# Performance work log

Measured on AMD Instinct MI355X. Metric: run time of the kernel, lower is better.

The kernel has to match this reference:

```python
import jax, jax.numpy as jnp
import numpy as np

B, T, F, C, H = 256, 96, 256, 256, 512
NH, FFD = 8, 64  # transformer nhead=8, dim_feedforward=64 (PyPOTS defaults)


def make_pe(L, d):
    pos = np.arange(L)[:, None].astype(np.float32)
    div = np.exp(np.arange(0, d, 2).astype(np.float32) * (-np.log(10000.0) / d))
    pe = np.zeros((L, d), np.float32)
    pe[:, 0::2] = np.sin(pos * div)
    pe[:, 1::2] = np.cos(pos * div)
    return jnp.asarray(pe)


def setup_inputs() -> dict:
    key = jax.random.key(0)
    it = iter(jax.random.split(key, 64))

    def u(shape):
        s = 1.0 / np.sqrt(shape[-1])
        return jax.random.uniform(next(it), shape, jnp.float32, -s, s)

    return {
        "x": jax.random.normal(next(it), (B, T, F), jnp.float32),
        "mask": (jax.random.uniform(next(it), (B, T, F)) > 0.3).astype(jnp.float32),
        "deltas": jax.random.uniform(next(it), (B, T, F), jnp.float32) * 5.0,
        "last_obs": jax.random.normal(next(it), (B, T, F), jnp.float32),
        "intervals": jax.random.uniform(next(it), (F,), jnp.float32) * 2.0,
        "Wo": u((F, F)), "bo": jnp.zeros(F),            # Decay_obs linear
        "Wip": u((C, F)), "bip": jnp.zeros(C),          # input_projection (k=1 conv)
        "Wqkv": u((3 * C, C)), "bqkv": jnp.zeros(3 * C),
        "Wao": u((C, C)), "bao": jnp.zeros(C),
        "g1": jnp.ones(C), "be1": jnp.zeros(C),
        "W1": u((FFD, C)), "b1": jnp.zeros(FFD),
        "W2": u((C, FFD)), "b2": jnp.zeros(C),
        "g2": jnp.ones(C), "be2": jnp.zeros(C),
        "Wop1": u((H, C)), "bop1": jnp.zeros(H),        # output_projection1
        "wop2": u((2 * T,)), "bop2": jnp.zeros(1),      # output_projection2 (2T->1, k=1)
        "Wdh": u((H, F)), "bdh": jnp.zeros(H),          # temp_decay_h
        "wdx": u((F,)), "bdx": jnp.zeros(F),            # temp_decay_x (diag)
        "Wh": u((F, H)), "bh": jnp.zeros(F),            # hist
        "Wfr": u((F, F)), "bfr": jnp.zeros(F),          # feat_reg_v (off-diag mask)
        "Wwc": u((F, 2 * F)), "bwc": jnp.zeros(F),      # weight_combine
        "Wih": u((3 * H, 2 * F)), "bih": jnp.zeros(3 * H),
        "Whh": u((3 * H, H)), "bhh": jnp.zeros(3 * H),
    }


def layernorm(x, g, b):
    mu = jnp.mean(x, -1, keepdims=True)
    v = jnp.var(x, -1, keepdims=True)
    return (x - mu) * jax.lax.rsqrt(v + 1e-5) * g + b


def _forward(x, mask, deltas, last_obs, intervals, Wo, bo, Wip, bip, Wqkv, bqkv,
             Wao, bao, g1, be1, W1, b1, W2, b2, g2, be2, Wop1, bop1, wop2, bop2,
             Wdh, bdh, wdx, bdx, Wh, bh, Wfr, bfr, Wwc, bwc, Wih, bih, Whh, bhh):
    Bb, Tt, Ff = x.shape
    Cc = Wip.shape[0]
    DH = Cc // NH
    # --- Decay_obs: weight = 0.5 * (1 - tanh(sign(dd) * |W dd + b|)) ---
    dd = deltas - intervals[None, None, :]
    wd = dd @ Wo.T + bo
    decay_factor = 0.5 * (1.0 - jnp.tanh(jnp.sign(dd) * jnp.abs(wd)))
    # --- pre-encoder (h is None path) ---
    pe = make_pe(Tt, Cc)[None]                      # (1, T, C)
    d_lo = last_obs @ Wip.T + bip + pe
    d_df = decay_factor @ Wip.T + bip + pe
    data = jnp.concatenate([d_lo, d_df], axis=1)    # (B, 2T, C)
    # TransformerEncoderLayer(batch_first=False) on (B, 2T, C):
    # seq dim = axis 0 (batch), "batch" dim = axis 1 -- faithful to source quirk.
    qkv = data @ Wqkv.T + bqkv
    q, k, v = jnp.split(qkv, 3, axis=-1)
    q = q.reshape(Bb, 2 * Tt, NH, DH)
    k = k.reshape(Bb, 2 * Tt, NH, DH)
    v = v.reshape(Bb, 2 * Tt, NH, DH)
    scores = jnp.einsum('ilhd,jlhd->lhij', q, k) / float(np.sqrt(DH))
    attn = jax.nn.softmax(scores, axis=-1)
    ctx = jnp.einsum('lhij,jlhd->ilhd', attn, v).reshape(Bb, 2 * Tt, Cc)
    data = layernorm(data + ctx @ Wao.T + bao, g1, be1)
    ff = jax.nn.gelu(data @ W1.T + b1, approximate=False) @ W2.T + b2
    data = layernorm(data + ff, g2, be2)
    data = data @ Wop1.T + bop1                     # (B, 2T, H)
    h0 = jnp.einsum('blh,l->bh', data, wop2) + bop2 # output_projection2 -> (B, H)
    # --- sequential imputation loop ---
    Wfr_m = Wfr * (1.0 - jnp.eye(Ff, dtype=Wfr.dtype))
    def step(h, ts):
        x_t, d_t, m_t = ts
        gamma_h = jnp.exp(-jax.nn.relu(d_t @ Wdh.T + bdh))
        h = h * gamma_h
        x_h = h @ Wh.T + bh
        x_r = m_t * x_t + (1.0 - m_t) * x_h
        xu = x_r @ Wfr_m.T + bfr
        gamma_x = jnp.exp(-jax.nn.relu(d_t * wdx + bdx))
        beta = jnp.concatenate([gamma_x, m_t], axis=-1) @ Wwc.T + bwc
        x_comb = beta * xu + (1.0 - beta) * x_h
        loss = jnp.sum(jnp.abs(x_comb - x_t) * m_t) / (jnp.sum(m_t) + 1e-12)
        x_imp_t = m_t * x_t + (1.0 - m_t) * x_comb
        gi = jnp.concatenate([x_imp_t, m_t], axis=-1) @ Wih.T + bih
        gh = h @ Whh.T + bhh
        ir, iz, inn = jnp.split(gi, 3, axis=-1)
        hr, hz, hn = jnp.split(gh, 3, axis=-1)
        r = jax.nn.sigmoid(ir + hr)
        z = jax.nn.sigmoid(iz + hz)
        n = jnp.tanh(inn + r * hn)
        h_new = (1.0 - z) * n + z * h
        return h_new, (x_imp_t, x_comb, loss)

    xs = (jnp.swapaxes(x, 0, 1), jnp.swapaxes(deltas, 0, 1), jnp.swapaxes(mask, 0, 1))
    h_fin, (xi, rec, losses) = jax.lax.scan(step, h0, xs)
    x_imp = jnp.swapaxes(xi, 0, 1)
    reconstruction = jnp.swapaxes(rec, 0, 1)
    return x_imp, reconstruction, h_fin, jnp.sum(losses)


def reference(x, mask, deltas, last_obs, intervals, Wo, bo, Wip, bip, Wqkv, bqkv,
              Wao, bao, g1, be1, W1, b1, W2, b2, g2, be2, Wop1, bop1, wop2, bop2,
              Wdh, bdh, wdx, bdx, Wh, bh, Wfr, bfr, Wwc, bwc, Wih, bih, Whh, bhh):
    return _forward(x, mask, deltas, last_obs, intervals, Wo, bo, Wip, bip, Wqkv,
                    bqkv, Wao, bao, g1, be1, W1, b1, W2, b2, g2, be2, Wop1, bop1,
                    wop2, bop2, Wdh, bdh, wdx, bdx, Wh, bh, Wfr, bfr, Wwc, bwc,
                    Wih, bih, Whh, bhh)
```

## Files before the change

### kernel.cpp

```cpp
#include <hip/hip_runtime.h>
#include <cstdint>
#include <cstddef>

#define DEV __device__ __forceinline__

typedef __attribute__((ext_vector_type(8))) short short8;
typedef __attribute__((ext_vector_type(4))) float f32x4;
typedef unsigned int uint;
typedef unsigned short ushort;

constexpr int Bb = 256, Tt = 96, Ff = 256, Cc = 256, Hh = 512;
constexpr int T2 = 192;

constexpr size_t SZ_DATA  = (size_t)Bb * T2 * Cc;
constexpr size_t SZ_QKV   = (size_t)Bb * T2 * 3 * Cc;
constexpr size_t OFF_DATA = 0;
constexpr size_t OFF_CTX  = OFF_DATA + SZ_DATA;
constexpr size_t OFF_QKV  = OFF_CTX + SZ_DATA;
constexpr size_t OFF_DF   = OFF_QKV;
constexpr size_t OFF_GAMH = OFF_QKV;
constexpr size_t OFF_BETA = OFF_QKV + (size_t)Bb * Tt * Hh;
constexpr size_t OFF_T1   = OFF_BETA + (size_t)Bb * Tt * Ff;
constexpr size_t OFF_S    = OFF_QKV + SZ_QKV;
constexpr size_t OFF_H    = OFF_S;
// ... 274 lines not shown
    }
  }
}

__global__ __launch_bounds__(256) void k_attnout(const float* __restrict__ ctx,
    const float* __restrict__ Wao, const float* __restrict__ bao, float* __restrict__ data) {
  mgemm<1>(256,
    [&](int m, int k) { return ctx[(size_t)m * 256 + k]; },
    [&](int g, int n, int k) { return Wao[(size_t)n * 256 + k]; },
    [&](float (&v)[1], int m, int n) {
      data[(size_t)m * 256 + n] += v[0] + bao[n];
    });
}

__global__ __launch_bounds__(256) void k_ln(float* __restrict__ data,
    const float* __restrict__ g, const float* __restrict__ b) {
  int row = blockIdx.x * 4 + (threadIdx.x >> 6);
  int lane = threadIdx.x & 63;
  float* p = data + (size_t)row * 256;
  float4 v = *(float4*)&p[lane * 4];
  float s = v.x + v.y + v.z + v.w;
  float q = v.x * v.x + v.y * v.y + v.z * v.z + v.w * v.w;
  for (int o = 32; o >= 1; o >>= 1) { s += __shfl_xor(s, o); q += __shfl_xor(q, o); }
  float mu = s * (1.f / 256.f);
  float var = q * (1.f / 256.f) - mu * mu;
  float inv = rsqrtf(var + 1e-5f);
  int c = lane * 4;
  v.x = (v.x - mu) * inv * g[c + 0] + b[c + 0];
  v.y = (v.y - mu) * inv * g[c + 1] + b[c + 1];
  v.z = (v.z - mu) * inv * g[c + 2] + b[c + 2];
  v.w = (v.w - mu) * inv * g[c + 3] + b[c + 3];
  *(float4*)&p[lane * 4] = v;
}

__global__ __launch_bounds__(256) void k_ff1(const float* __restrict__ data,
    const float* __restrict__ W1, const float* __restrict__ b1, float* __restrict__ t1) {
  mgemm<1>(256,
    [&](int m, int k) { return data[(size_t)m * 256 + k]; },
    [&](int g, int n, int k) { return W1[(size_t)n * 256 + k]; },
    [&](float (&v)[1], int m, int n) {
      float u = v[0] + b1[n];
      u = 0.5f * u * (1.f + erff(u * 0.7071067811865476f));
      t1[(size_t)m * 64 + n] = u;
    });
}

__global__ __launch_bounds__(256) void k_ff2(const float* __restrict__ t1,
    const float* __restrict__ W2, const float* __restrict__ b2, float* __restrict__ data) {
  mgemm<1>(64,
    [&](int m, int k) { return t1[(size_t)m * 64 + k]; },
    [&](int g, int n, int k) { return W2[(size_t)n * 64 + k]; },
    [&](float (&v)[1], int m, int n) {
      data[(size_t)m * 256 + n] += v[0] + b2[n];
    });
}

__global__ __launch_bounds__(256) void k_dbar(const float* __restrict__ data,
    const float* __restrict__ wop2, float* __restrict__ dbar, float* __restrict__ sw) {
  int b = blockIdx.x, c = threadIdx.x;
  float acc = 0.f;
  for (int lq = 0; lq < 192; lq++) acc += wop2[lq] * data[((size_t)b * 192 + lq) * 256 + c];
  dbar[(size_t)b * 256 + c] = acc;
  if (b == 0 && c == 0) {
    float s = 0.f;
    for (int lq = 0; lq < 192; lq++) s += wop2[lq];
    sw[0] = s;
  }
}

__global__ __launch_bounds__(256) void k_h0(const float* __restrict__ dbar,
    const float* __restrict__ Wop1, const float* __restrict__ bop1,
    const float* __restrict__ bop2, const float* __restrict__ sw, float* __restrict__ h) {
  mgemm<1>(256,
    [&](int m, int k) { return dbar[(size_t)m * 256 + k]; },
    [&](int g, int n, int k) { return Wop1[(size_t)n * 256 + k]; },
    [&](float (&v)[1], int m, int n) {
      h[(size_t)m * 512 + n] = v[0] + sw[0] * bop1[n] + bop2[0];
    });
}

__global__ __launch_bounds__(256) void k_gamh(const float* __restrict__ deltas,
    const float* __restrict__ Wdh, const float* __restrict__ bdh, float* __restrict__ gamH) {
  mgemm<1>(256,
    [&](int m, int k) { return deltas[(size_t)m * 256 + k]; },
    [&](int g, int n, int k) { return Wdh[(size_t)n * 256 + k]; },
    [&](float (&v)[1], int m, int n) {
      gamH[(size_t)m * 512 + n] = __expf(-fmaxf(v[0] + bdh[n], 0.f));
    });
}

__global__ __launch_bounds__(256) void k_beta(const float* __restrict__ deltas,
    const float* __restrict__ mask, const float* __restrict__ wdx, const float* __restrict__ bdx,
    const float* __restrict__ Wwc, const float* __restrict__ bwc, float* __restrict__ beta) {
  mgemm<1>(512,
    [&](int m, int k) {
      if (k < 256) {
        float d = deltas[(size_t)m * 256 + k];
        return __expf(-fmaxf(fmaf(d, wdx[k], bdx[k]), 0.f));
      }
      return mask[(size_t)m * 256 + (k - 256)];
    },
    [&](int g, int n, int k) { return Wwc[(size_t)n * 512 + k]; },
    [&](float (&v)[1], int m, int n) {
      beta[(size_t)m * 256 + n] = v[0] + bwc[n];
    });
}

__global__ __launch_bounds__(256) void k_den(const float* __restrict__ mask, float* __restrict__ den) {
  int t = blockIdx.x, tid = threadIdx.x;
  float s = 0.f;
  for (int idx = tid; idx < 256 * 256; idx += 256) {
    int b = idx >> 8, f = idx & 255;
    s += mask[((size_t)b * 96 + t) * 256 + f];
  }
  for (int o = 32; o >= 1; o >>= 1) s += __shfl_xor(s, o);
  __shared__ float rs[4];
  if ((tid & 63) == 0) rs[tid >> 6] = s;
  __syncthreads();
  if (tid == 0) den[t] = rs[0] + rs[1] + rs[2] + rs[3] + 1e-12f;
}

__global__ __launch_bounds__(256) void k_splitB1(const float* __restrict__ Wh,
    const float* __restrict__ Whh, ushort* __restrict__ ph, ushort* __restrict__ plo) {
  int i = blockIdx.x * 256 + threadIdx.x;
  int n = i >> 9, k = i & 511;
  float v = (n < 256) ? Wh[(size_t)n * 512 + k] : Whh[(size_t)(n - 256) * 512 + k];
  ushort hb = f2bf(v);
  ph[i] = hb; plo[i] = f2bf(v - bf2f(hb));
}
__global__ __launch_bounds__(256) void k_splitB2(const float* __restrict__ Wfr,
    ushort* __restrict__ ph, ushort* __restrict__ plo) {
  int i = blockIdx.x * 256 + threadIdx.x;
  int n = i >> 8, k = i & 255;
  float v = (n == k) ? 0.f : Wfr[i];
  ushort hb = f2bf(v);
  ph[i] = hb; plo[i] = f2bf(v - bf2f(hb));
}
__global__ __launch_bounds__(256) void k_splitB3(const float* __restrict__ Wih,
    ushort* __restrict__ ph, ushort* __restrict__ plo) {
  int i = blockIdx.x * 256 + threadIdx.x;
  float v = Wih[i];
  ushort hb = f2bf(v);
  ph[i] = hb; plo[i] = f2bf(v - bf2f(hb));
}
__global__ __launch_bounds__(256) void k_initA(const float* __restrict__ h,
    const float* __restrict__ gamH, ushort* __restrict__ ah, ushort* __restrict__ al) {
  int i = blockIdx.x * 256 + threadIdx.x;
  int m = i >> 9, k = i & 511;
  float v = h[i] * gamH[(size_t)m * 49152 + k];
  ushort hb = f2bf(v);
  ah[i] = hb; al[i] = f2bf(v - bf2f(hb));
}


__global__ __launch_bounds__(256) void k_lp1(const ushort* __restrict__ pl,
    float* __restrict__ xh, float* __restrict__ gh) {
  const int bid = blockIdx.x, tid = threadIdx.x;
  const int w = tid >> 6, l = tid & 63;
  const ushort* B1h = pl + U_B1H; const ushort* B1l = pl + U_B1L;
  const ushort* Ah  = pl + U_AH;  const ushort* Al  = pl + U_AL;
  __shared__ __align__(16) ushort As[64][64];
  __shared__ __align__(16) ushort Bs[64][64];
  const int fr = l & 15, fc = l >> 4;
  const int em = (w << 4) + (fc << 2);
  const int sr = tid >> 2, sc = tid & 3;
  const int hsS = sc ^ (sr & 7);
  const int m0 = (bid / 28) * 64, n0 = (bid % 28) * 64;

  const ushort* pAh = Ah + (size_t)(m0 + sr) * 512 + sc * 8;
  const ushort* pAl = Al + (size_t)(m0 + sr) * 512 + sc * 8;
  const ushort* pBh = B1h + (size_t)(n0 + sr) * 512 + sc * 8;
  const ushort* pBl = B1l + (size_t)(n0 + sr) * 512 + sc * 8;
  short8 rah = *(const short8*)pAh, ral = *(const short8*)pAl;
  short8 rbh = *(const short8*)pBh, rbl = *(const short8*)pBl;
  f32x4 acc[4];
#pragma unroll
  for (int i = 0; i < 4; i++) acc[i] = (f32x4){0.f, 0.f, 0.f, 0.f};
  for (int ks = 0; ks < 16; ks++) {
    __syncthreads();
    *(short8*)&As[sr][hsS * 8] = rah;
    *(short8*)&As[sr][(hsS ^ 4) * 8] = ral;
    *(short8*)&Bs[sr][hsS * 8] = rbh;
    *(short8*)&Bs[sr][(hsS ^ 4) * 8] = rbl;
    __syncthreads();
    if (ks < 15) {
      int ko = (ks + 1) * 32;
      rah = *(const short8*)(pAh + ko); ral = *(const short8*)(pAl + ko);
      rbh = *(const short8*)(pBh + ko); rbl = *(const short8*)(pBl + ko);
    }
    int r = (w << 4) + fr; int ha = fc ^ (r & 7);
    short8 avh = *(const short8*)&As[r][ha * 8];
    short8 avl = *(const short8*)&As[r][(ha ^ 4) * 8];
#pragma unroll
    for (int nb = 0; nb < 4; nb++) {
      int br = (nb << 4) + fr; int hb = fc ^ (br & 7);
      short8 bvh = *(const short8*)&Bs[br][hb * 8];
      short8 bvl = *(const short8*)&Bs[br][(hb ^ 4) * 8];
      f32x4 a = acc[nb];
      a = __builtin_amdgcn_mfma_f32_16x16x32_bf16(avh, bvh, a, 0, 0, 0);
      a = __builtin_amdgcn_mfma_f32_16x16x32_bf16(avh, bvl, a, 0, 0, 0);
      a = __builtin_amdgcn_mfma_f32_16x16x32_bf16(avl, bvh, a, 0, 0, 0);
      acc[nb] = a;
    }
  }
#pragma unroll
  for (int nb = 0; nb < 4; nb++)
#pragma unroll
    for (int reg = 0; reg < 4; reg++) {
      int m = m0 + em + reg, n = n0 + (nb << 4) + fr;
      float v = acc[nb][reg];
      if (n < 256) xh[(size_t)m * 256 + n] = v;
      else gh[(size_t)m * 1536 + (n - 256)] = v;
    }
}

__global__ __launch_bounds__(256) void k_lp2(ushort* __restrict__ pl,
    const float* __restrict__ xh, const float* __restrict__ x, const float* __restrict__ mask,
    const float* __restrict__ beta, const float* __restrict__ bh, const float* __restrict__ bfr,
    float* __restrict__ out_ximp, float* __restrict__ out_rec,
    float* __restrict__ lossp, int t) {
  const int bid = blockIdx.x, tid = threadIdx.x;
  const int w = tid >> 6, l = tid & 63;
  const ushort* B2h = pl + U_B2H; const ushort* B2l = pl + U_B2L;
  ushort* Xih = pl + U_XIH; ushort* Xil = pl + U_XIL;
  __shared__ __align__(16) ushort As[64][64];
  __shared__ __align__(16) ushort Bs[64][64];
  __shared__ float rs[4];
  const int fr = l & 15, fc = l >> 4;
  const int em = (w << 4) + (fc << 2);
  const int sr = tid >> 2, sc = tid & 3;
  const int hsS = sc ^ (sr & 7);
  const int m0 = (bid >> 2) * 64, n0 = (bid & 3) * 64;

  const ushort* pBh = B2h + (size_t)(n0 + sr) * 256 + sc * 8;
  const ushort* pBl = B2l + (size_t)(n0 + sr) * 256 + sc * 8;
  float am[8], ax[8], ahv[8], ab[8];
  auto ldA = [&](int kc) {
    size_t base = ((size_t)(m0 + sr) * 96 + t) * 256 + kc * 32 + sc * 8;
    float4 a0 = *(const float4*)(mask + base), a1 = *(const float4*)(mask + base + 4);
    float4 b0 = *(const float4*)(x + base),    b1 = *(const float4*)(x + base + 4);
    size_t hb_ = (size_t)(m0 + sr) * 256 + kc * 32 + sc * 8;
    float4 c0 = *(const float4*)(xh + hb_),    c1 = *(const float4*)(xh + hb_ + 4);
    const float* pb = bh + kc * 32 + sc * 8;
    float4 d0 = *(const float4*)pb,            d1 = *(const float4*)(pb + 4);
    am[0]=a0.x; am[1]=a0.y; am[2]=a0.z; am[3]=a0.w; am[4]=a1.x; am[5]=a1.y; am[6]=a1.z; am[7]=a1.w;
    ax[0]=b0.x; ax[1]=b0.y; ax[2]=b0.z; ax[3]=b0.w; ax[4]=b1.x; ax[5]=b1.y; ax[6]=b1.z; ax[7]=b1.w;
    ahv[0]=c0.x; ahv[1]=c0.y; ahv[2]=c0.z; ahv[3]=c0.w; ahv[4]=c1.x; ahv[5]=c1.y; ahv[6]=c1.z; ahv[7]=c1.w;
    ab[0]=d0.x; ab[1]=d0.y; ab[2]=d0.z; ab[3]=d0.w; ab[4]=d1.x; ab[5]=d1.y; ab[6]=d1.z; ab[7]=d1.w;
  };
  ldA(0);
  f32x4 acc[4];
#pragma unroll
  for (int i = 0; i < 4; i++) acc[i] = (f32x4){0.f, 0.f, 0.f, 0.f};
  for (int ks = 0; ks < 8; ks++) {
    short8 hv, lv;
#pragma unroll
    for (int j = 0; j < 8; j++) {
      float v = am[j] * ax[j] + (1.f - am[j]) * (ahv[j] + ab[j]);
      ushort hb2 = f2bf(v);
      hv[j] = (short)hb2; lv[j] = (short)f2bf(v - bf2f(hb2));
    }
    __syncthreads();
    *(short8*)&As[sr][hsS * 8] = hv;
    *(short8*)&As[sr][(hsS ^ 4) * 8] = lv;
    *(short8*)&Bs[sr][hsS * 8] = *(const short8*)(pBh + ks * 32);
    *(short8*)&Bs[sr][(hsS ^ 4) * 8] = *(const short8*)(pBl + ks * 32);
    __syncthreads();
    if (ks < 7) ldA(ks + 1);
    int r = (w << 4) + fr; int ha = fc ^ (r & 7);
    short8 avh = *(const short8*)&As[r][ha * 8];
    short8 avl = *(const short8*)&As[r][(ha ^ 4) * 8];
#pragma unroll
    for (int nb = 0; nb < 4; nb++) {
      int br = (nb << 4) + fr; int hb = fc ^ (br & 7);
      short8 bvh = *(const short8*)&Bs[br][hb * 8];
      short8 bvl = *(const short8*)&Bs[br][(hb ^ 4) * 8];
      f32x4 a = acc[nb];
      a = __builtin_amdgcn_mfma_f32_16x16x32_bf16(avh, bvh, a, 0, 0, 0);
      a = __builtin_amdgcn_mfma_f32_16x16x32_bf16(avh, bvl, a, 0, 0, 0);
      a = __builtin_amdgcn_mfma_f32_16x16x32_bf16(avl, bvh, a, 0, 0, 0);
      acc[nb] = a;
    }
  }
  float lsum = 0.f;
#pragma unroll
  for (int nb = 0; nb < 4; nb++)
#pragma unroll
    for (int reg = 0; reg < 4; reg++) {
      int m = m0 + em + reg, n = n0 + (nb << 4) + fr;
      size_t i3 = ((size_t)m * 96 + t) * 256 + n;
      float xu = acc[nb][reg] + bfr[n];
      float xhv = xh[(size_t)m * 256 + n] + bh[n];
      float bt = beta[i3];
      float xc = bt * xu + (1.f - bt) * xhv;
      float mk = mask[i3], xv = x[i3];
      float xim = mk * xv + (1.f - mk) * xc;
      out_ximp[i3] = xim;
      out_rec[i3] = xc;
      ushort hb2 = f2bf(xim);
      Xih[(size_t)m * 256 + n] = hb2;
      Xil[(size_t)m * 256 + n] = f2bf(xim - bf2f(hb2));
      lsum += fabsf(xc - xv) * mk;
    }
  for (int o = 32; o >= 1; o >>= 1) lsum += __shfl_xor(lsum, o);
  if ((tid & 63) == 0) rs[tid >> 6] = lsum;
  __syncthreads();
  if (tid == 0) lossp[bid] = rs[0] + rs[1] + rs[2] + rs[3];
}

__global__ __launch_bounds__(256) void k_lp3(ushort* __restrict__ pl,
    const float* __restrict__ mask, const float* __restrict__ gamH,
    const float* __restrict__ gh, const float* __restrict__ bih,
    const float* __restrict__ bhh, float* __restrict__ h,
    const float* __restrict__ lossp, float* __restrict__ lossacc,
    const float* __restrict__ den, int t) {
  const int bid = blockIdx.x, tid = threadIdx.x;
  const int w = tid >> 6, l = tid & 63;
  const ushort* B3h = pl + U_B3H; const ushort* B3l = pl + U_B3L;
  const ushort* Xih = pl + U_XIH; const ushort* Xil = pl + U_XIL;
  ushort* Ah = pl + U_AH; ushort* Al = pl + U_AL;
  __shared__ __align__(16) ushort As[64][64];
  __shared__ __align__(16) ushort Bs[6144];
  const int fr = l & 15, fc = l >> 4;
  const int em = (w << 4) + (fc << 2);
  const int sr = tid >> 2, sc = tid & 3;
  const int hsS = sc ^ (sr & 7);
  const int row3 = tid >> 3, c3 = (tid >> 1) & 3, pl3 = tid & 1;
  const int hsB3 = (c3 ^ (row3 & 7)) ^ (pl3 ? 4 : 0);
  const int m0 = (bid >> 4) * 64, j0 = (bid & 15) * 32;

  if (bid == 0 && tid == 0) {
    float s = 0.f;
    for (int i = 0; i < 16; i++) s += lossp[i];
    lossacc[0] += s / den[t];
  }

  const ushort* pB = pl3 ? B3l : B3h;
  f32x4 acc[3][2];
#pragma unroll
  for (int g = 0; g < 3; g++)
#pragma unroll
    for (int nb = 0; nb < 2; nb++) acc[g][nb] = (f32x4){0.f, 0.f, 0.f, 0.f};
  short8 rA_h, rA_l, rB0, rB1, rB2;
  {
    rA_h = *(const short8*)(Xih + (size_t)(m0 + sr) * 256 + sc * 8);
    rA_l = *(const short8*)(Xil + (size_t)(m0 + sr) * 256 + sc * 8);
    rB0 = *(const short8*)(pB + (size_t)(j0 + row3) * 512 + c3 * 8);
    rB1 = *(const short8*)(pB + (size_t)(512 + j0 + row3) * 512 + c3 * 8);
    rB2 = *(const short8*)(pB + (size_t)(1024 + j0 + row3) * 512 + c3 * 8);
  }
  for (int ks = 0; ks < 16; ks++) {
    __syncthreads();
    *(short8*)&As[sr][hsS * 8] = rA_h;
    *(short8*)&As[sr][(hsS ^ 4) * 8] = rA_l;
    *(short8*)&Bs[(0 * 32 + row3) * 64 + hsB3 * 8] = rB0;
    *(short8*)&Bs[(1 * 32 + row3) * 64 + hsB3 * 8] = rB1;
    *(short8*)&Bs[(2 * 32 + row3) * 64 + hsB3 * 8] = rB2;
    __syncthreads();
    if (ks < 15) {
      int ko = (ks + 1) * 32;
      if (ko < 256) {
        rA_h = *(const short8*)(Xih + (size_t)(m0 + sr) * 256 + ko + sc * 8);
        rA_l = *(const short8*)(Xil + (size_t)(m0 + sr) * 256 + ko + sc * 8);
      } else {
        const float* pm = mask + ((size_t)(m0 + sr) * 96 + t) * 256 + (ko - 256) + sc * 8;
        short8 hv;
#pragma unroll
        for (int j = 0; j < 8; j++) hv[j] = (short)f2bf(pm[j]);
        rA_h = hv;
        rA_l = (short8){0, 0, 0, 0, 0, 0, 0, 0};
      }
      rB0 = *(const short8*)(pB + (size_t)(j0 + row3) * 512 + ko + c3 * 8);
      rB1 = *(const short8*)(pB + (size_t)(512 + j0 + row3) * 512 + ko + c3 * 8);
      rB2 = *(const short8*)(pB + (size_t)(1024 + j0 + row3) * 512 + ko + c3 * 8);
    }
    int r = (w << 4) + fr; int ha = fc ^ (r & 7);
    short8 avh = *(const short8*)&As[r][ha * 8];
    short8 avl = *(const short8*)&As[r][(ha ^ 4) * 8];
#pragma unroll
    for (int nb = 0; nb < 2; nb++) {
      int br = (nb << 4) + fr; int hb = fc ^ (br & 7);
#pragma unroll
      for (int g = 0; g < 3; g++) {
        short8 bvh = *(const short8*)&Bs[(g * 32 + br) * 64 + hb * 8];
        short8 bvl = *(const short8*)&Bs[(g * 32 + br) * 64 + (hb ^ 4) * 8];
        f32x4 a = acc[g][nb];
        a = __builtin_amdgcn_mfma_f32_16x16x32_bf16(avh, bvh, a, 0, 0, 0);
        a = __builtin_amdgcn_mfma_f32_16x16x32_bf16(avh, bvl, a, 0, 0, 0);
        a = __builtin_amdgcn_mfma_f32_16x16x32_bf16(avl, bvh, a, 0, 0, 0);
        acc[g][nb] = a;
      }
    }
  }
#pragma unroll
  for (int nb = 0; nb < 2; nb++)
#pragma unroll
    for (int reg = 0; reg < 4; reg++) {
      int m = m0 + em + reg, j = j0 + (nb << 4) + fr;
      size_t gb = (size_t)m * 1536 + j;
      float r_ = sigmoidf_(acc[0][nb][reg] + bih[j] + gh[gb] + bhh[j]);
      float z_ = sigmoidf_(acc[1][nb][reg] + bih[512 + j] + gh[gb + 512] + bhh[512 + j]);
      float n_ = tanhf(acc[2][nb][reg] + bih[1024 + j] + r_ * (gh[gb + 1024] + bhh[1024 + j]));
      size_t hidx = (size_t)m * 512 + j;
      float hd = bf2f(Ah[hidx]) + bf2f(Al[hidx]);
      float hnew = (1.f - z_) * n_ + z_ * hd;
      h[hidx] = hnew;
      if (t < 95) {
        float an = hnew * gamH[((size_t)m * 96 + t + 1) * 512 + j];
        ushort hb2 = f2bf(an);
        Ah[hidx] = hb2;
        Al[hidx] = f2bf(an - bf2f(hb2));
      }
    }
}

extern "C" void kernel_launch(void* const* d_in, const int* in_sizes, int n_in,
                              void* d_out, int out_size, void* d_ws, size_t ws_size,
                              hipStream_t stream) {
  if (ws_size < WS_FLOATS * sizeof(float)) return;

  const float* x        = (const float*)d_in[0];
  const float* mask     = (const float*)d_in[1];
  const float* deltas   = (const float*)d_in[2];
  const float* last_obs = (const float*)d_in[3];
  const float* intervals= (const float*)d_in[4];
  const float* Wo  = (const float*)d_in[5];
  const float* bo  = (const float*)d_in[6];
  const float* Wip = (const float*)d_in[7];
  const float* bip = (const float*)d_in[8];
  const float* Wqkv= (const float*)d_in[9];
  const float* bqkv= (const float*)d_in[10];
  const float* Wao = (const float*)d_in[11];
  const float* bao = (const float*)d_in[12];
  const float* g1  = (const float*)d_in[13];
  const float* be1 = (const float*)d_in[14];
  const float* W1  = (const float*)d_in[15];
  const float* b1  = (const float*)d_in[16];
  const float* W2  = (const float*)d_in[17];
  const float* b2  = (const float*)d_in[18];
  const float* g2  = (const float*)d_in[19];
  const float* be2 = (const float*)d_in[20];
  const float* Wop1= (const float*)d_in[21];
  const float* bop1= (const float*)d_in[22];
  const float* wop2= (const float*)d_in[23];
  const float* bop2= (const float*)d_in[24];
  const float* Wdh = (const float*)d_in[25];
  const float* bdh = (const float*)d_in[26];
  const float* wdx = (const float*)d_in[27];
  const float* bdx = (const float*)d_in[28];
  const float* Wh  = (const float*)d_in[29];
  const float* bh  = (const float*)d_in[30];
  const float* Wfr = (const float*)d_in[31];
  const float* bfr = (const float*)d_in[32];
  const float* Wwc = (const float*)d_in[33];
  const float* bwc = (const float*)d_in[34];
  const float* Wih = (const float*)d_in[35];
  const float* bih = (const float*)d_in[36];
  const float* Whh = (const float*)d_in[37];
  const float* bhh = (const float*)d_in[38];

  float* out = (float*)d_out;
  float* ws  = (float*)d_ws;
  float* data  = ws + OFF_DATA;
  float* ctx   = ws + OFF_CTX;
  float* qkv   = ws + OFF_QKV;
  float* df    = ws + OFF_DF;
  float* gamH  = ws + OFF_GAMH;
  float* beta  = ws + OFF_BETA;
  float* t1    = ws + OFF_T1;
  float* h     = ws + OFF_H;
  float* dbar  = ws + OFF_DBAR;
  float* xh    = ws + OFF_XH;
  float* gh    = ws + OFF_GH;
  float* lossp = ws + OFF_LOSSP;
  float* den   = ws + OFF_DEN;
  float* sw    = ws + OFF_SW;
  float* lossacc = ws + OFF_LOSS;
  ushort* plz  = (ushort*)(ws + OFF_CTX);

  float* out_ximp = out;
  float* out_rec  = out + (size_t)Bb * Tt * Ff;
  float* out_h    = out + 2 * (size_t)Bb * Tt * Ff;
  float* out_loss = out_h + (size_t)Bb * Hh;

  const dim3 blk(256);

  k_decay<<<dim3(4, 192), blk, 0, stream>>>(deltas, intervals, Wo, bo, df);
  k_proj<<<dim3(4, 192), blk, 0, stream>>>(last_obs, Wip, bip, data, 0);
  k_proj<<<dim3(4, 192), blk, 0, stream>>>(df, Wip, bip, data, 1);
  k_qkv<<<dim3(12, 384), blk, 0, stream>>>(data, Wqkv, bqkv, qkv);
  k_attn<<<dim3(6144), blk, 0, stream>>>(qkv, ctx);
  k_attnout<<<dim3(4, 768), blk, 0, stream>>>(ctx, Wao, bao, data);
  k_splitB1<<<dim3(3584), blk, 0, stream>>>(Wh, Whh, plz + U_B1H, plz + U_B1L);
  k_splitB2<<<dim3(256), blk, 0, stream>>>(Wfr, plz + U_B2H, plz + U_B2L);
  k_splitB3<<<dim3(3072), blk, 0, stream>>>(Wih, plz + U_B3H, plz + U_B3L);
  k_ln<<<dim3(12288), blk, 0, stream>>>(data, g1, be1);
  k_ff1<<<dim3(1, 384), blk, 0, stream>>>(data, W1, b1, t1);
  k_ff2<<<dim3(4, 384), blk, 0, stream>>>(t1, W2, b2, data);
  k_ln<<<dim3(12288), blk, 0, stream>>>(data, g2, be2);
  k_dbar<<<dim3(256), blk, 0, stream>>>(data, wop2, dbar, sw);
  k_h0<<<dim3(8, 2), blk, 0, stream>>>(dbar, Wop1, bop1, bop2, sw, h);

  k_gamh<<<dim3(8, 192), blk, 0, stream>>>(deltas, Wdh, bdh, gamH);
  k_beta<<<dim3(4, 192), blk, 0, stream>>>(deltas, mask, wdx, bdx, Wwc, bwc, beta);
  k_den<<<dim3(96), blk, 0, stream>>>(mask, den);
  k_initA<<<dim3(512), blk, 0, stream>>>(h, gamH, plz + U_AH, plz + U_AL);
  hipMemsetAsync(lossacc, 0, sizeof(float), stream);

  for (int t = 0; t < 96; t++) {
    k_lp1<<<dim3(112), blk, 0, stream>>>(plz, xh, gh);
    k_lp2<<<dim3(16), blk, 0, stream>>>(plz, xh, x, mask, beta, bh, bfr,
                                        out_ximp, out_rec, lossp, t);
    k_lp3<<<dim3(64), blk, 0, stream>>>(plz, mask, gamH, gh, bih, bhh, h,
                                        lossp, lossacc, den, t);
  }

  hipMemcpyAsync(out_h, h, (size_t)Bb * Hh * sizeof(float), hipMemcpyDeviceToDevice, stream);
  hipMemcpyAsync(out_loss, lossacc, sizeof(float), hipMemcpyDeviceToDevice, stream);
}
```

Measured before the change: 5.423 ms.

## Fuse per-step recurrent kernels into one launch with flag-based inter-block sync

Merges the three per-timestep kernels (hidden projection GEMM, feature regression, GRU gate GEMM) into a single 112-block kernel. Inter-stage dependencies are enforced with per-tile release/acquire flags and a counter in global memory, so later stages wait only on the producer tiles they need. This cuts two launches and two full grid barriers per step over 96 steps. It relies on all 112 blocks being co-resident to avoid deadlock, and adds spin-wait overhead.

```diff
diff --git a/kernel.cpp b/kernel.cpp
--- a/kernel.cpp
+++ b/kernel.cpp
@@ -450,266 +450,288 @@
   ah[i] = hb; al[i] = f2bf(v - bf2f(hb));
 }
 
-
-__global__ __launch_bounds__(256) void k_lp1(const ushort* __restrict__ pl,
-    float* __restrict__ xh, float* __restrict__ gh) {
+__global__ __launch_bounds__(256) void k_step(
+    ushort* __restrict__ pl, float* __restrict__ xh, float* __restrict__ gh,
+    const float* __restrict__ x, const float* __restrict__ mask,
+    const float* __restrict__ gamH, const float* __restrict__ beta,
+    const float* __restrict__ den, const float* __restrict__ bh,
+    const float* __restrict__ bfr, const float* __restrict__ bih,
+    const float* __restrict__ bhh, float* __restrict__ h,
+    float* __restrict__ out_ximp, float* __restrict__ out_rec,
+    float* __restrict__ lossp, float* __restrict__ lossacc,
+    uint* __restrict__ flags, int t) {
   const int bid = blockIdx.x, tid = threadIdx.x;
   const int w = tid >> 6, l = tid & 63;
   const ushort* B1h = pl + U_B1H; const ushort* B1l = pl + U_B1L;
-  const ushort* Ah  = pl + U_AH;  const ushort* Al  = pl + U_AL;
+  const ushort* B3h = pl + U_B3H; const ushort* B3l = pl + U_B3L;
+  const ushort* B2h = pl + U_B2H; const ushort* B2l = pl + U_B2L;
+  ushort* Ah  = pl + U_AH;  ushort* Al  = pl + U_AL;
+  ushort* Xih = pl + U_XIH; ushort* Xil = pl + U_XIL;
+  uint* flag1 = flags;
+  uint* flag2 = flags + 1792;
+  uint* cnt2  = flags + 2048;
+
   __shared__ __align__(16) ushort As[64][64];
-  __shared__ __align__(16) ushort Bs[64][64];
+  __shared__ __align__(16) ushort Bs[6144];
+  __shared__ float rs[4];
+
   const int fr = l & 15, fc = l >> 4;
   const int em = (w << 4) + (fc << 2);
   const int sr = tid >> 2, sc = tid & 3;
   const int hsS = sc ^ (sr & 7);
-  const int m0 = (bid / 28) * 64, n0 = (bid % 28) * 64;
-
-  const ushort* pAh = Ah + (size_t)(m0 + sr) * 512 + sc * 8;
-  const ushort* pAl = Al + (size_t)(m0 + sr) * 512 + sc * 8;
-  const ushort* pBh = B1h + (size_t)(n0 + sr) * 512 + sc * 8;
-  const ushort* pBl = B1l + (size_t)(n0 + sr) * 512 + sc * 8;
-  short8 rah = *(const short8*)pAh, ral = *(const short8*)pAl;
-  short8 rbh = *(const short8*)pBh, rbl = *(const short8*)pBl;
-  f32x4 acc[4];
-#pragma unroll
-  for (int i = 0; i < 4; i++) acc[i] = (f32x4){0.f, 0.f, 0.f, 0.f};
-  for (int ks = 0; ks < 16; ks++) {
-    __syncthreads();
-    *(short8*)&As[sr][hsS * 8] = rah;
-    *(short8*)&As[sr][(hsS ^ 4) * 8] = ral;
-    *(short8*)&Bs[sr][hsS * 8] = rbh;
-    *(short8*)&Bs[sr][(hsS ^ 4) * 8] = rbl;
-    __syncthreads();
-    if (ks < 15) {
-      int ko = (ks + 1) * 32;
-      rah = *(const short8*)(pAh + ko); ral = *(const short8*)(pAl + ko);
-      rbh = *(const short8*)(pBh + ko); rbl = *(const short8*)(pBl + ko);
-    }
-    int r = (w << 4) + fr; int ha = fc ^ (r & 7);
-    short8 avh = *(const short8*)&As[r][ha * 8];
-    short8 avl = *(const short8*)&As[r][(ha ^ 4) * 8];
-#pragma unroll
-    for (int nb = 0; nb < 4; nb++) {
-      int br = (nb << 4) + fr; int hb = fc ^ (br & 7);
-      short8 bvh = *(const short8*)&Bs[br][hb * 8];
-      short8 bvl = *(const short8*)&Bs[br][(hb ^ 4) * 8];
-      f32x4 a = acc[nb];
-      a = __builtin_amdgcn_mfma_f32_16x16x32_bf16(avh, bvh, a, 0, 0, 0);
-      a = __builtin_amdgcn_mfma_f32_16x16x32_bf16(avh, bvl, a, 0, 0, 0);
-      a = __builtin_amdgcn_mfma_f32_16x16x32_bf16(avl, bvh, a, 0, 0, 0);
-      acc[nb] = a;
-    }
-  }
-#pragma unroll
-  for (int nb = 0; nb < 4; nb++)
-#pragma unroll
-    for (int reg = 0; reg < 4; reg++) {
-      int m = m0 + em + reg, n = n0 + (nb << 4) + fr;
-      float v = acc[nb][reg];
-      if (n < 256) xh[(size_t)m * 256 + n] = v;
-      else gh[(size_t)m * 1536 + (n - 256)] = v;
-    }
-}
-
-__global__ __launch_bounds__(256) void k_lp2(ushort* __restrict__ pl,
-    const float* __restrict__ xh, const float* __restrict__ x, const float* __restrict__ mask,
-    const float* __restrict__ beta, const float* __restrict__ bh, const float* __restrict__ bfr,
-    float* __restrict__ out_ximp, float* __restrict__ out_rec,
-    float* __restrict__ lossp, int t) {
-  const int bid = blockIdx.x, tid = threadIdx.x;
-  const int w = tid >> 6, l = tid & 63;
-  const ushort* B2h = pl + U_B2H; const ushort* B2l = pl + U_B2L;
-  ushort* Xih = pl + U_XIH; ushort* Xil = pl + U_XIL;
-  __shared__ __align__(16) ushort As[64][64];
-  __shared__ __align__(16) ushort Bs[64][64];
-  __shared__ float rs[4];
-  const int fr = l & 15, fc = l >> 4;
-  const int em = (w << 4) + (fc << 2);
-  const int sr = tid >> 2, sc = tid & 3;
-  const int hsS = sc ^ (sr & 7);
-  const int m0 = (bid >> 2) * 64, n0 = (bid & 3) * 64;
-
-  const ushort* pBh = B2h + (size_t)(n0 + sr) * 256 + sc * 8;
-  const ushort* pBl = B2l + (size_t)(n0 + sr) * 256 + sc * 8;
-  float am[8], ax[8], ahv[8], ab[8];
-  auto ldA = [&](int kc) {
-    size_t base = ((size_t)(m0 + sr) * 96 + t) * 256 + kc * 32 + sc * 8;
-    float4 a0 = *(const float4*)(mask + base), a1 = *(const float4*)(mask + base + 4);
-    float4 b0 = *(const float4*)(x + base),    b1 = *(const float4*)(x + base + 4);
-    size_t hb_ = (size_t)(m0 + sr) * 256 + kc * 32 + sc * 8;
-    float4 c0 = *(const float4*)(xh + hb_),    c1 = *(const float4*)(xh + hb_ + 4);
-    const float* pb = bh + kc * 32 + sc * 8;
-    float4 d0 = *(const float4*)pb,            d1 = *(const float4*)(pb + 4);
-    am[0]=a0.x; am[1]=a0.y; am[2]=a0.z; am[3]=a0.w; am[4]=a1.x; am[5]=a1.y; am[6]=a1.z; am[7]=a1.w;
-    ax[0]=b0.x; ax[1]=b0.y; ax[2]=b0.z; ax[3]=b0.w; ax[4]=b1.x; ax[5]=b1.y; ax[6]=b1.z; ax[7]=b1.w;
-    ahv[0]=c0.x; ahv[1]=c0.y; ahv[2]=c0.z; ahv[3]=c0.w; ahv[4]=c1.x; ahv[5]=c1.y; ahv[6]=c1.z; ahv[7]=c1.w;
-    ab[0]=d0.x; ab[1]=d0.y; ab[2]=d0.z; ab[3]=d0.w; ab[4]=d1.x; ab[5]=d1.y; ab[6]=d1.z; ab[7]=d1.w;
-  };
-  ldA(0);
-  f32x4 acc[4];
-#pragma unroll
-  for (int i = 0; i < 4; i++) acc[i] = (f32x4){0.f, 0.f, 0.f, 0.f};
-  for (int ks = 0; ks < 8; ks++) {
-    short8 hv, lv;
-#pragma unroll
-    for (int j = 0; j < 8; j++) {
-      float v = am[j] * ax[j] + (1.f - am[j]) * (ahv[j] + ab[j]);
-      ushort hb2 = f2bf(v);
-      hv[j] = (short)hb2; lv[j] = (short)f2bf(v - bf2f(hb2));
-    }
-    __syncthreads();
-    *(short8*)&As[sr][hsS * 8] = hv;
-    *(short8*)&As[sr][(hsS ^ 4) * 8] = lv;
-    *(short8*)&Bs[sr][hsS * 8] = *(const short8*)(pBh + ks * 32);
-    *(short8*)&Bs[sr][(hsS ^ 4) * 8] = *(const short8*)(pBl + ks * 32);
-    __syncthreads();
-    if (ks < 7) ldA(ks + 1);
-    int r = (w << 4) + fr; int ha = fc ^ (r & 7);
-    short8 avh = *(const short8*)&As[r][ha * 8];
-    short8 avl = *(const short8*)&As[r][(ha ^ 4) * 8];
-#pragma unroll
-    for (int nb = 0; nb < 4; nb++) {
-      int br = (nb << 4) + fr; int hb = fc ^ (br & 7);
-      short8 bvh = *(const short8*)&Bs[br][hb * 8];
-      short8 bvl = *(const short8*)&Bs[br][(hb ^ 4) * 8];
-      f32x4 a = acc[nb];
-      a = __builtin_amdgcn_mfma_f32_16x16x32_bf16(avh, bvh, a, 0, 0, 0);
-      a = __builtin_amdgcn_mfma_f32_16x16x32_bf16(avh, bvl, a, 0, 0, 0);
-      a = __builtin_amdgcn_mfma_f32_16x16x32_bf16(avl, bvh, a, 0, 0, 0);
-      acc[nb] = a;
-    }
-  }
-  float lsum = 0.f;
-#pragma unroll
-  for (int nb = 0; nb < 4; nb++)
-#pragma unroll
-    for (int reg = 0; reg < 4; reg++) {
-      int m = m0 + em + reg, n = n0 + (nb << 4) + fr;
-      size_t i3 = ((size_t)m * 96 + t) * 256 + n;
-      float xu = acc[nb][reg] + bfr[n];
-      float xhv = xh[(size_t)m * 256 + n] + bh[n];
-      float bt = beta[i3];
-      float xc = bt * xu + (1.f - bt) * xhv;
-      float mk = mask[i3], xv = x[i3];
-      float xim = mk * xv + (1.f - mk) * xc;
-      out_ximp[i3] = xim;
-      out_rec[i3] = xc;
-      ushort hb2 = f2bf(xim);
-      Xih[(size_t)m * 256 + n] = hb2;
-      Xil[(size_t)m * 256 + n] = f2bf(xim - bf2f(hb2));
-      lsum += fabsf(xc - xv) * mk;
-    }
-  for (int o = 32; o >= 1; o >>= 1) lsum += __shfl_xor(lsum, o);
-  if ((tid & 63) == 0) rs[tid >> 6] = lsum;
-  __syncthreads();
-  if (tid == 0) lossp[bid] = rs[0] + rs[1] + rs[2] + rs[3];
-}
-
-__global__ __launch_bounds__(256) void k_lp3(ushort* __restrict__ pl,
-    const float* __restrict__ mask, const float* __restrict__ gamH,
-    const float* __restrict__ gh, const float* __restrict__ bih,
-    const float* __restrict__ bhh, float* __restrict__ h,
-    const float* __restrict__ lossp, float* __restrict__ lossacc,
-    const float* __restrict__ den, int t) {
-  const int bid = blockIdx.x, tid = threadIdx.x;
-  const int w = tid >> 6, l = tid & 63;
-  const ushort* B3h = pl + U_B3H; const ushort* B3l = pl + U_B3L;
-  const ushort* Xih = pl + U_XIH; const ushort* Xil = pl + U_XIL;
-  ushort* Ah = pl + U_AH; ushort* Al = pl + U_AL;
-  __shared__ __align__(16) ushort As[64][64];
-  __shared__ __align__(16) ushort Bs[6144];
-  const int fr = l & 15, fc = l >> 4;
-  const int em = (w << 4) + (fc << 2);
-  const int sr = tid >> 2, sc = tid & 3;
-  const int hsS = sc ^ (sr & 7);
-  const int row3 = tid >> 3, c3 = (tid >> 1) & 3, pl3 = tid & 1;
-  const int hsB3 = (c3 ^ (row3 & 7)) ^ (pl3 ? 4 : 0);
-  const int m0 = (bid >> 4) * 64, j0 = (bid & 15) * 32;
-
-  if (bid == 0 && tid == 0) {
-    float s = 0.f;
-    for (int i = 0; i < 16; i++) s += lossp[i];
-    lossacc[0] += s / den[t];
-  }
-
-  const ushort* pB = pl3 ? B3l : B3h;
-  f32x4 acc[3][2];
-#pragma unroll
-  for (int g = 0; g < 3; g++)
-#pragma unroll
-    for (int nb = 0; nb < 2; nb++) acc[g][nb] = (f32x4){0.f, 0.f, 0.f, 0.f};
-  short8 rA_h, rA_l, rB0, rB1, rB2;
+  const uint tgt = (uint)(t + 1);
+
   {
-    rA_h = *(const short8*)(Xih + (size_t)(m0 + sr) * 256 + sc * 8);
-    rA_l = *(const short8*)(Xil + (size_t)(m0 + sr) * 256 + sc * 8);
-    rB0 = *(const short8*)(pB + (size_t)(j0 + row3) * 512 + c3 * 8);
-    rB1 = *(const short8*)(pB + (size_t)(512 + j0 + row3) * 512 + c3 * 8);
-    rB2 = *(const short8*)(pB + (size_t)(1024 + j0 + row3) * 512 + c3 * 8);
-  }
-  for (int ks = 0; ks < 16; ks++) {
-    __syncthreads();
-    *(short8*)&As[sr][hsS * 8] = rA_h;
-    *(short8*)&As[sr][(hsS ^ 4) * 8] = rA_l;
-    *(short8*)&Bs[(0 * 32 + row3) * 64 + hsB3 * 8] = rB0;
-    *(short8*)&Bs[(1 * 32 + row3) * 64 + hsB3 * 8] = rB1;
-    *(short8*)&Bs[(2 * 32 + row3) * 64 + hsB3 * 8] = rB2;
-    __syncthreads();
-    if (ks < 15) {
-      int ko = (ks + 1) * 32;
-      if (ko < 256) {
-        rA_h = *(const short8*)(Xih + (size_t)(m0 + sr) * 256 + ko + sc * 8);
-        rA_l = *(const short8*)(Xil + (size_t)(m0 + sr) * 256 + ko + sc * 8);
-      } else {
-        const float* pm = mask + ((size_t)(m0 + sr) * 96 + t) * 256 + (ko - 256) + sc * 8;
-        short8 hv;
-#pragma unroll
-        for (int j = 0; j < 8; j++) hv[j] = (short)f2bf(pm[j]);
-        rA_h = hv;
-        rA_l = (short8){0, 0, 0, 0, 0, 0, 0, 0};
-      }
-      rB0 = *(const short8*)(pB + (size_t)(j0 + row3) * 512 + ko + c3 * 8);
-      rB1 = *(const short8*)(pB + (size_t)(512 + j0 + row3) * 512 + ko + c3 * 8);
-      rB2 = *(const short8*)(pB + (size_t)(1024 + j0 + row3) * 512 + ko + c3 * 8);
-    }
-    int r = (w << 4) + fr; int ha = fc ^ (r & 7);
-    short8 avh = *(const short8*)&As[r][ha * 8];
-    short8 avl = *(const short8*)&As[r][(ha ^ 4) * 8];
-#pragma unroll
-    for (int nb = 0; nb < 2; nb++) {
-      int br = (nb << 4) + fr; int hb = fc ^ (br & 7);
-#pragma unroll
-      for (int g = 0; g < 3; g++) {
-        short8 bvh = *(const short8*)&Bs[(g * 32 + br) * 64 + hb * 8];
-        short8 bvl = *(const short8*)&Bs[(g * 32 + br) * 64 + (hb ^ 4) * 8];
-        f32x4 a = acc[g][nb];
+    const int m0 = (bid / 28) * 64, n0 = (bid % 28) * 64;
+    const ushort* pAh = Ah + (size_t)(m0 + sr) * 512 + sc * 8;
+    const ushort* pAl = Al + (size_t)(m0 + sr) * 512 + sc * 8;
+    const ushort* pBh = B1h + (size_t)(n0 + sr) * 512 + sc * 8;
+    const ushort* pBl = B1l + (size_t)(n0 + sr) * 512 + sc * 8;
+    short8 rah = *(const short8*)pAh, ral = *(const short8*)pAl;
+    short8 rbh = *(const short8*)pBh, rbl = *(const short8*)pBl;
+    f32x4 acc[4];
+#pragma unroll
+    for (int i = 0; i < 4; i++) acc[i] = (f32x4){0.f, 0.f, 0.f, 0.f};
+    for (int ks = 0; ks < 16; ks++) {
+      __syncthreads();
+      *(short8*)&As[sr][hsS * 8] = rah;
+      *(short8*)&As[sr][(hsS ^ 4) * 8] = ral;
+      *(short8*)&Bs[sr * 64 + hsS * 8] = rbh;
+      *(short8*)&Bs[sr * 64 + (hsS ^ 4) * 8] = rbl;
+      __syncthreads();
+      if (ks < 15) {
+        int ko = (ks + 1) * 32;
+        rah = *(const short8*)(pAh + ko); ral = *(const short8*)(pAl + ko);
+        rbh = *(const short8*)(pBh + ko); rbl = *(const short8*)(pBl + ko);
+      }
+      int r = (w << 4) + fr; int ha = fc ^ (r & 7);
+      short8 avh = *(const short8*)&As[r][ha * 8];
+      short8 avl = *(const short8*)&As[r][(ha ^ 4) * 8];
+#pragma unroll
+      for (int nb = 0; nb < 4; nb++) {
+        int br = (nb << 4) + fr; int hb = fc ^ (br & 7);
+        short8 bvh = *(const short8*)&Bs[br * 64 + hb * 8];
+        short8 bvl = *(const short8*)&Bs[br * 64 + (hb ^ 4) * 8];
+        f32x4 a = acc[nb];
         a = __builtin_amdgcn_mfma_f32_16x16x32_bf16(avh, bvh, a, 0, 0, 0);
         a = __builtin_amdgcn_mfma_f32_16x16x32_bf16(avh, bvl, a, 0, 0, 0);
         a = __builtin_amdgcn_mfma_f32_16x16x32_bf16(avl, bvh, a, 0, 0, 0);
-        acc[g][nb] = a;
-      }
-    }
-  }
-#pragma unroll
-  for (int nb = 0; nb < 2; nb++)
-#pragma unroll
-    for (int reg = 0; reg < 4; reg++) {
-      int m = m0 + em + reg, j = j0 + (nb << 4) + fr;
-      size_t gb = (size_t)m * 1536 + j;
-      float r_ = sigmoidf_(acc[0][nb][reg] + bih[j] + gh[gb] + bhh[j]);
-      float z_ = sigmoidf_(acc[1][nb][reg] + bih[512 + j] + gh[gb + 512] + bhh[512 + j]);
-      float n_ = tanhf(acc[2][nb][reg] + bih[1024 + j] + r_ * (gh[gb + 1024] + bhh[1024 + j]));
-      size_t hidx = (size_t)m * 512 + j;
-      float hd = bf2f(Ah[hidx]) + bf2f(Al[hidx]);
-      float hnew = (1.f - z_) * n_ + z_ * hd;
-      h[hidx] = hnew;
-      if (t < 95) {
-        float an = hnew * gamH[((size_t)m * 96 + t + 1) * 512 + j];
-        ushort hb2 = f2bf(an);
-        Ah[hidx] = hb2;
-        Al[hidx] = f2bf(an - bf2f(hb2));
-      }
-    }
+        acc[nb] = a;
+      }
+    }
+#pragma unroll
+    for (int nb = 0; nb < 4; nb++)
+#pragma unroll
+      for (int reg = 0; reg < 4; reg++) {
+        int m = m0 + em + reg, n = n0 + (nb << 4) + fr;
+        float v = acc[nb][reg];
+        if (n < 256) xh[(size_t)m * 256 + n] = v;
+        else gh[(size_t)m * 1536 + (n - 256)] = v;
+      }
+  }
+  __syncthreads();
+  if (tid == 0) {
+    __threadfence();
+    __hip_atomic_store(&flag1[bid * 16], tgt, __ATOMIC_RELEASE, __HIP_MEMORY_SCOPE_AGENT);
+  }
+
+  if (bid < 16) {
+    const int m0 = (bid >> 2) * 64, n0 = (bid & 3) * 64;
+    const int mt = bid >> 2;
+    if (tid == 0) {
+      for (int i = 0; i < 4; i++)
+        while (__hip_atomic_load(&flag1[(mt * 28 + i) * 16], __ATOMIC_ACQUIRE,
+                                 __HIP_MEMORY_SCOPE_AGENT) < tgt)
+          __builtin_amdgcn_s_sleep(1);
+      __threadfence();
+    }
+    __syncthreads();
+
+    const ushort* pBh = B2h + (size_t)(n0 + sr) * 256 + sc * 8;
+    const ushort* pBl = B2l + (size_t)(n0 + sr) * 256 + sc * 8;
+    float am[8], ax[8], ahv[8], ab[8];
+    auto ldA = [&](int kc) {
+      size_t base = ((size_t)(m0 + sr) * 96 + t) * 256 + kc * 32 + sc * 8;
+      float4 a0 = *(const float4*)(mask + base), a1 = *(const float4*)(mask + base + 4);
+      float4 b0 = *(const float4*)(x + base),    b1 = *(const float4*)(x + base + 4);
+      size_t hb_ = (size_t)(m0 + sr) * 256 + kc * 32 + sc * 8;
+      float4 c0 = *(const float4*)(xh + hb_),    c1 = *(const float4*)(xh + hb_ + 4);
+      const float* pb = bh + kc * 32 + sc * 8;
+      float4 d0 = *(const float4*)pb,            d1 = *(const float4*)(pb + 4);
+      am[0]=a0.x; am[1]=a0.y; am[2]=a0.z; am[3]=a0.w; am[4]=a1.x; am[5]=a1.y; am[6]=a1.z; am[7]=a1.w;
+      ax[0]=b0.x; ax[1]=b0.y; ax[2]=b0.z; ax[3]=b0.w; ax[4]=b1.x; ax[5]=b1.y; ax[6]=b1.z; ax[7]=b1.w;
+      ahv[0]=c0.x; ahv[1]=c0.y; ahv[2]=c0.z; ahv[3]=c0.w; ahv[4]=c1.x; ahv[5]=c1.y; ahv[6]=c1.z; ahv[7]=c1.w;
+      ab[0]=d0.x; ab[1]=d0.y; ab[2]=d0.z; ab[3]=d0.w; ab[4]=d1.x; ab[5]=d1.y; ab[6]=d1.z; ab[7]=d1.w;
+    };
+    ldA(0);
+    f32x4 acc[4];
+#pragma unroll
+    for (int i = 0; i < 4; i++) acc[i] = (f32x4){0.f, 0.f, 0.f, 0.f};
+    for (int ks = 0; ks < 8; ks++) {
+      short8 hv, lv;
+#pragma unroll
+      for (int j = 0; j < 8; j++) {
+        float v = am[j] * ax[j] + (1.f - am[j]) * (ahv[j] + ab[j]);
+        ushort hb2 = f2bf(v);
+        hv[j] = (short)hb2; lv[j] = (short)f2bf(v - bf2f(hb2));
+      }
+      __syncthreads();
+      *(short8*)&As[sr][hsS * 8] = hv;
+      *(short8*)&As[sr][(hsS ^ 4) * 8] = lv;
+      *(short8*)&Bs[sr * 64 + hsS * 8] = *(const short8*)(pBh + ks * 32);
+      *(short8*)&Bs[sr * 64 + (hsS ^ 4) * 8] = *(const short8*)(pBl + ks * 32);
+      __syncthreads();
+      if (ks < 7) ldA(ks + 1);
+      int r = (w << 4) + fr; int ha = fc ^ (r & 7);
+      short8 avh = *(const short8*)&As[r][ha * 8];
+      short8 avl = *(const short8*)&As[r][(ha ^ 4) * 8];
+#pragma unroll
+      for (int nb = 0; nb < 4; nb++) {
+        int br = (nb << 4) + fr; int hb = fc ^ (br & 7);
+        short8 bvh = *(const short8*)&Bs[br * 64 + hb * 8];
+        short8 bvl = *(const short8*)&Bs[br * 64 + (hb ^ 4) * 8];
+        f32x4 a = acc[nb];
+        a = __builtin_amdgcn_mfma_f32_16x16x32_bf16(avh, bvh, a, 0, 0, 0);
+        a = __builtin_amdgcn_mfma_f32_16x16x32_bf16(avh, bvl, a, 0, 0, 0);
+        a = __builtin_amdgcn_mfma_f32_16x16x32_bf16(avl, bvh, a, 0, 0, 0);
+        acc[nb] = a;
+      }
+    }
+    float lsum = 0.f;
+#pragma unroll
+    for (int nb = 0; nb < 4; nb++)
+#pragma unroll
+      for (int reg = 0; reg < 4; reg++) {
+        int m = m0 + em + reg, n = n0 + (nb << 4) + fr;
+        size_t i3 = ((size_t)m * 96 + t) * 256 + n;
+        float xu = acc[nb][reg] + bfr[n];
+        float xhv = xh[(size_t)m * 256 + n] + bh[n];
+        float bt = beta[i3];
+        float xc = bt * xu + (1.f - bt) * xhv;
+        float mk = mask[i3], xv = x[i3];
+        float xim = mk * xv + (1.f - mk) * xc;
+        out_ximp[i3] = xim;
+        out_rec[i3] = xc;
+        ushort hb2 = f2bf(xim);
+        Xih[(size_t)m * 256 + n] = hb2;
+        Xil[(size_t)m * 256 + n] = f2bf(xim - bf2f(hb2));
+        lsum += fabsf(xc - xv) * mk;
+      }
+    for (int o = 32; o >= 1; o >>= 1) lsum += __shfl_xor(lsum, o);
+    if ((tid & 63) == 0) rs[tid >> 6] = lsum;
+    __syncthreads();
+    if (tid == 0) {
+      lossp[bid] = rs[0] + rs[1] + rs[2] + rs[3];
+      __threadfence();
+      __hip_atomic_store(&flag2[bid * 16], tgt, __ATOMIC_RELEASE, __HIP_MEMORY_SCOPE_AGENT);
+      uint old = __hip_atomic_fetch_add(cnt2, 1u, __ATOMIC_ACQ_REL, __HIP_MEMORY_SCOPE_AGENT);
+      if (old == (uint)(16 * t + 15)) {
+        float s = 0.f;
+        for (int i = 0; i < 16; i++) s += lossp[i];
+        lossacc[0] += s / den[t];
+      }
+    }
+  }
+
+  if (bid >= 16 && bid < 80) {
+    const int q = bid - 16;
+    const int m0 = (q >> 4) * 64, j0 = (q & 15) * 32;
+    const int mt = q >> 4;
+    if (tid == 0) {
+      const int nta = 4 + (j0 >> 6), ntb = 12 + (j0 >> 6), ntc = 20 + (j0 >> 6);
+      while (__hip_atomic_load(&flag1[(mt * 28 + nta) * 16], __ATOMIC_ACQUIRE,
+                               __HIP_MEMORY_SCOPE_AGENT) < tgt) __builtin_amdgcn_s_sleep(1);
+      while (__hip_atomic_load(&flag1[(mt * 28 + ntb) * 16], __ATOMIC_ACQUIRE,
+                               __HIP_MEMORY_SCOPE_AGENT) < tgt) __builtin_amdgcn_s_sleep(1);
+      while (__hip_atomic_load(&flag1[(mt * 28 + ntc) * 16], __ATOMIC_ACQUIRE,
+                               __HIP_MEMORY_SCOPE_AGENT) < tgt) __builtin_amdgcn_s_sleep(1);
+      for (int i = 0; i < 4; i++)
+        while (__hip_atomic_load(&flag2[(mt * 4 + i) * 16], __ATOMIC_ACQUIRE,
+                                 __HIP_MEMORY_SCOPE_AGENT) < tgt) __builtin_amdgcn_s_sleep(1);
+      __threadfence();
+    }
+    __syncthreads();
+
+    const int row3 = tid >> 3, c3 = (tid >> 1) & 3, pl3 = tid & 1;
+    const int hsB3 = (c3 ^ (row3 & 7)) ^ (pl3 ? 4 : 0);
+    const ushort* pB = pl3 ? B3l : B3h;
+    f32x4 acc[3][2];
+#pragma unroll
+    for (int g = 0; g < 3; g++)
+#pragma unroll
+      for (int nb = 0; nb < 2; nb++) acc[g][nb] = (f32x4){0.f, 0.f, 0.f, 0.f};
+    short8 rA_h, rA_l, rB0, rB1, rB2;
+    {
+      rA_h = *(const short8*)(Xih + (size_t)(m0 + sr) * 256 + sc * 8);
+      rA_l = *(const short8*)(Xil + (size_t)(m0 + sr) * 256 + sc * 8);
+      rB0 = *(const short8*)(pB + (size_t)(j0 + row3) * 512 + c3 * 8);
+      rB1 = *(const short8*)(pB + (size_t)(512 + j0 + row3) * 512 + c3 * 8);
+      rB2 = *(const short8*)(pB + (size_t)(1024 + j0 + row3) * 512 + c3 * 8);
+    }
+    for (int ks = 0; ks < 16; ks++) {
+      __syncthreads();
+      *(short8*)&As[sr][hsS * 8] = rA_h;
+      *(short8*)&As[sr][(hsS ^ 4) * 8] = rA_l;
+      *(short8*)&Bs[(0 * 32 + row3) * 64 + hsB3 * 8] = rB0;
+      *(short8*)&Bs[(1 * 32 + row3) * 64 + hsB3 * 8] = rB1;
+      *(short8*)&Bs[(2 * 32 + row3) * 64 + hsB3 * 8] = rB2;
+      __syncthreads();
+      if (ks < 15) {
+        int ko = (ks + 1) * 32;
+        if (ko < 256) {
+          rA_h = *(const short8*)(Xih + (size_t)(m0 + sr) * 256 + ko + sc * 8);
+          rA_l = *(const short8*)(Xil + (size_t)(m0 + sr) * 256 + ko + sc * 8);
+        } else {
+          const float* pm = mask + ((size_t)(m0 + sr) * 96 + t) * 256 + (ko - 256) + sc * 8;
+          short8 hv;
+#pragma unroll
+          for (int j = 0; j < 8; j++) hv[j] = (short)f2bf(pm[j]);
+          rA_h = hv;
+          rA_l = (short8){0, 0, 0, 0, 0, 0, 0, 0};
+        }
+        rB0 = *(const short8*)(pB + (size_t)(j0 + row3) * 512 + ko + c3 * 8);
+        rB1 = *(const short8*)(pB + (size_t)(512 + j0 + row3) * 512 + ko + c3 * 8);
+        rB2 = *(const short8*)(pB + (size_t)(1024 + j0 + row3) * 512 + ko + c3 * 8);
+      }
+      int r = (w << 4) + fr; int ha = fc ^ (r & 7);
+      short8 avh = *(const short8*)&As[r][ha * 8];
+      short8 avl = *(const short8*)&As[r][(ha ^ 4) * 8];
+#pragma unroll
+      for (int nb = 0; nb < 2; nb++) {
+        int br = (nb << 4) + fr; int hb = fc ^ (br & 7);
+#pragma unroll
+        for (int g = 0; g < 3; g++) {
+          short8 bvh = *(const short8*)&Bs[(g * 32 + br) * 64 + hb * 8];
+          short8 bvl = *(const short8*)&Bs[(g * 32 + br) * 64 + (hb ^ 4) * 8];
+          f32x4 a = acc[g][nb];
+          a = __builtin_amdgcn_mfma_f32_16x16x32_bf16(avh, bvh, a, 0, 0, 0);
+          a = __builtin_amdgcn_mfma_f32_16x16x32_bf16(avh, bvl, a, 0, 0, 0);
+          a = __builtin_amdgcn_mfma_f32_16x16x32_bf16(avl, bvh, a, 0, 0, 0);
+          acc[g][nb] = a;
+        }
+      }
+    }
+#pragma unroll
+    for (int nb = 0; nb < 2; nb++)
+#pragma unroll
+      for (int reg = 0; reg < 4; reg++) {
+        int m = m0 + em + reg, j = j0 + (nb << 4) + fr;
+        size_t gb = (size_t)m * 1536 + j;
+        float r_ = sigmoidf_(acc[0][nb][reg] + bih[j] + gh[gb] + bhh[j]);
+        float z_ = sigmoidf_(acc[1][nb][reg] + bih[512 + j] + gh[gb + 512] + bhh[512 + j]);
+        float n_ = tanhf(acc[2][nb][reg] + bih[1024 + j] + r_ * (gh[gb + 1024] + bhh[1024 + j]));
+        size_t hidx = (size_t)m * 512 + j;
+        float hd = bf2f(Ah[hidx]) + bf2f(Al[hidx]);
+        float hnew = (1.f - z_) * n_ + z_ * hd;
+        h[hidx] = hnew;
+        if (t < 95) {
+          float an = hnew * gamH[((size_t)m * 96 + t + 1) * 512 + j];
+          ushort hb2 = f2bf(an);
+          Ah[hidx] = hb2;
+          Al[hidx] = f2bf(an - bf2f(hb2));
+        }
+      }
+  }
 }
 
 extern "C" void kernel_launch(void* const* d_in, const int* in_sizes, int n_in,
@@ -774,6 +796,7 @@
   float* den   = ws + OFF_DEN;
   float* sw    = ws + OFF_SW;
   float* lossacc = ws + OFF_LOSS;
+  uint*  flags = (uint*)(ws + OFF_XI);
   ushort* plz  = (ushort*)(ws + OFF_CTX);
 
   float* out_ximp = out;
@@ -804,13 +827,13 @@
   k_den<<<dim3(96), blk, 0, stream>>>(mask, den);
   k_initA<<<dim3(512), blk, 0, stream>>>(h, gamH, plz + U_AH, plz + U_AL);
   hipMemsetAsync(lossacc, 0, sizeof(float), stream);
+  hipMemsetAsync(flags, 0, 2080 * sizeof(uint), stream);
 
   for (int t = 0; t < 96; t++) {
-    k_lp1<<<dim3(112), blk, 0, stream>>>(plz, xh, gh);
-    k_lp2<<<dim3(16), blk, 0, stream>>>(plz, xh, x, mask, beta, bh, bfr,
-                                        out_ximp, out_rec, lossp, t);
-    k_lp3<<<dim3(64), blk, 0, stream>>>(plz, mask, gamH, gh, bih, bhh, h,
-                                        lossp, lossacc, den, t);
+    k_step<<<dim3(112), blk, 0, stream>>>(plz, xh, gh, x, mask, gamH, beta, den,
+                                          bh, bfr, bih, bhh, h,
+                                          out_ximp, out_rec, lossp, lossacc,
+                                          flags, t);
   }
 
   hipMemcpyAsync(out_h, h, (size_t)Bb * Hh * sizeof(float), hipMemcpyDeviceToDevice, stream);
```

Result: slower. 7.992 ms (+47.4%).
